# Performance work log

Measured on AMD Instinct MI355X. Metric: run time of the kernel, lower is better.

The kernel has to match this reference:

```python
import jax, jax.numpy as jnp
import numpy as np

N, E, IN_DIM, HID, G, NCLS, LAYERS = 200000, 1200000, 128, 64, 1024, 6, 3
BN_EPS = 1e-5


def _bn(x, g, b, m, v):
    # eval-mode BatchNorm1d with running stats
    return (x - m) * jax.lax.rsqrt(v + BN_EPS) * g + b


def setup_inputs() -> dict:
    key = jax.random.key(0)
    ks = jax.random.split(key, 24)
    s = 0.05
    d = {
        "x": jax.random.normal(ks[0], (N, IN_DIM), jnp.float32),
        "edge_index": jax.random.randint(ks[1], (2, E), 0, N, dtype=jnp.int32),
        "batch": jnp.sort(jax.random.randint(ks[2], (N,), 0, G, dtype=jnp.int32)),
        # input embedding + input BN
        "emb_w": jax.random.normal(ks[3], (IN_DIM, HID), jnp.float32) * s,
        "emb_b": jnp.zeros((HID,), jnp.float32),
        "ibn_g": jnp.ones((HID,), jnp.float32),
        "ibn_b": jnp.zeros((HID,), jnp.float32),
        "ibn_m": jax.random.normal(ks[4], (HID,), jnp.float32) * 0.1,
        "ibn_v": jax.random.uniform(ks[5], (HID,), jnp.float32, 0.5, 1.5),
        # stacked per-layer GIN MLP params [LAYERS, ...]
        "fc1_w": jax.random.normal(ks[6], (LAYERS, HID, HID), jnp.float32) * s,
        "fc1_b": jnp.zeros((LAYERS, HID), jnp.float32),
        "mbn_g": jnp.ones((LAYERS, HID), jnp.float32),
        "mbn_b": jnp.zeros((LAYERS, HID), jnp.float32),
        "mbn_m": jax.random.normal(ks[7], (LAYERS, HID), jnp.float32) * 0.1,
        "mbn_v": jax.random.uniform(ks[8], (LAYERS, HID), jnp.float32, 0.5, 1.5),
        "fc2_w": jax.random.normal(ks[9], (LAYERS, HID, HID), jnp.float32) * s,
        "fc2_b": jnp.zeros((LAYERS, HID), jnp.float32),
        # stacked per-layer outer BN params
        "obn_g": jnp.ones((LAYERS, HID), jnp.float32),
        "obn_b": jnp.zeros((LAYERS, HID), jnp.float32),
        "obn_m": jax.random.normal(ks[10], (LAYERS, HID), jnp.float32) * 0.1,
        "obn_v": jax.random.uniform(ks[11], (LAYERS, HID), jnp.float32, 0.5, 1.5),
        # classifier head
        "cls1_w": jax.random.normal(ks[12], (HID, HID // 2), jnp.float32) * s,
        "cls1_b": jnp.zeros((HID // 2,), jnp.float32),
        "cls2_w": jax.random.normal(ks[13], (HID // 2, NCLS), jnp.float32) * s,
        "cls2_b": jnp.zeros((NCLS,), jnp.float32),
    }
    return d


def reference(x, edge_index, batch,
              emb_w, emb_b, ibn_g, ibn_b, ibn_m, ibn_v,
              fc1_w, fc1_b, mbn_g, mbn_b, mbn_m, mbn_v, fc2_w, fc2_b,
              obn_g, obn_b, obn_m, obn_v,
              cls1_w, cls1_b, cls2_w, cls2_b):
    n = x.shape[0]
    src, dst = edge_index[0], edge_index[1]

    # input embed -> BN -> relu (dropout = identity in eval)
    h = jnp.dot(x, emb_w) + emb_b
    h = jax.nn.relu(_bn(h, ibn_g, ibn_b, ibn_m, ibn_v))

    for i in range(LAYERS):
        # GINConv (eps=0): aggregate neighbors via scatter-add, then MLP
        agg = jax.ops.segment_sum(h[src], dst, num_segments=n)
        z = h + agg
        z = jnp.dot(z, fc1_w[i]) + fc1_b[i]
        z = jax.nn.relu(_bn(z, mbn_g[i], mbn_b[i], mbn_m[i], mbn_v[i]))
        z = jnp.dot(z, fc2_w[i]) + fc2_b[i]
        # outer BN + relu
        h = jax.nn.relu(_bn(z, obn_g[i], obn_b[i], obn_m[i], obn_v[i]))

    # global mean pool per graph
    sums = jax.ops.segment_sum(h, batch, num_segments=G)
    cnts = jax.ops.segment_sum(jnp.ones((n,), h.dtype), batch, num_segments=G)
    pooled = sums / jnp.maximum(cnts, 1.0)[:, None]

    # classifier
    out = jax.nn.relu(jnp.dot(pooled, cls1_w) + cls1_b)
    out = jnp.dot(out, cls2_w) + cls2_b
    return out
```

## Files before the change

### kernel.cpp

```cpp
#include <hip/hip_runtime.h>
#include <hip/hip_bf16.h>

#define N_NODES 200000
#define N_EDGES 1200000
#define IN_DIM  128
#define HID     64
#define NGRAPH  1024
#define NCLS    6
#define BN_EPS  1e-5f

#define TILE_N   64
#define ZS       68
#define ECAP     1024

#define SCAN_CHUNK 1024
#define NBLK_SCAN ((N_NODES + SCAN_CHUNK - 1) / SCAN_CHUNK)

#define NBKT   128
#define BRANGE 1568
#define BCAP   12288
#define EPB    4096
#define NB_BIN ((N_EDGES + EPB - 1) / EPB)

#define SWZ(s) ((s) ^ (((s) >> 4) & 3))

typedef short bf16x8 __attribute__((ext_vector_type(8)));
typedef float f32x4  __attribute__((ext_vector_type(4)));
#define MFMA16(a,b,c) __builtin_amdgcn_mfma_f32_16x16x32_bf16((a),(b),(c),0,0,0)

__device__ __forceinline__ unsigned short f2bf(float f) {
    union { __hip_bfloat16 h; unsigned short u; } v; v.h = __float2bfloat16(f); return v.u;
}
__device__ __forceinline__ float bfbits2f(unsigned short u) {
    union { unsigned int i; float f; } v; v.i = ((unsigned int)u) << 16; return v.f;
}
__device__ __forceinline__ void cvt4(const float4& x, uint2& hi, uint2& lo) {
    const unsigned short h0 = f2bf(x.x), h1 = f2bf(x.y), h2 = f2bf(x.z), h3 = f2bf(x.w);
    hi.x = (unsigned)h0 | ((unsigned)h1 << 16);
    hi.y = (unsigned)h2 | ((unsigned)h3 << 16);
    const unsigned short l0 = f2bf(x.x - bfbits2f(h0)), l1 = f2bf(x.y - bfbits2f(h1));
    const unsigned short l2 = f2bf(x.z - bfbits2f(h2)), l3 = f2bf(x.w - bfbits2f(h3));
    lo.x = (unsigned)l0 | ((unsigned)l1 << 16);
    lo.y = (unsigned)l2 | ((unsigned)l3 << 16);
}

__global__ __launch_bounds__(256) void prep_emb_kernel(
    const float* __restrict__ w, unsigned short* __restrict__ wpe)
{
    const int idx = blockIdx.x * 256 + threadIdx.x;
    if (idx >= 16384) return;
    const int j = idx & 7, l = (idx >> 3) & 63;
    const int plane = (idx >> 9) & 1, s = (idx >> 10) & 3, ct = (idx >> 12) & 3;
    const int n = ct * 16 + (l & 15);
    const int k = s * 32 + (l >> 4) * 8 + j;
    const float f = w[k * 64 + n];
    const unsigned short hb = f2bf(f);
    wpe[idx] = plane ? f2bf(f - bfbits2f(hb)) : hb;
}

__global__ __launch_bounds__(256) void prep_fc_kernel(
    const float* __restrict__ fc1, const float* __restrict__ fc2,
    unsigned short* __restrict__ wpf)
{
    const int idx = blockIdx.x * 256 + threadIdx.x;
    if (idx >= 49152) return;
    const int j = idx & 7, l = (idx >> 3) & 63;
    const int plane = (idx >> 9) & 1, s = (idx >> 10) & 1, ct = (idx >> 11) & 3;
    const int g = (idx >> 13) & 1, layer = idx >> 14;
    const int n = ct * 16 + (l & 15);
    const int k = s * 32 + (l >> 4) * 8 + j;
    const float* W = g ? fc2 : fc1;
    const float f = W[(layer * 64 + k) * 64 + n];
    const unsigned short hb = f2bf(f);
    wpf[idx] = plane ? f2bf(f - bfbits2f(hb)) : hb;
}

__global__ __launch_bounds__(256) void bin_kernel(
    const int* __restrict__ src, const int* __restrict__ dst,
    int* __restrict__ gcnt, uint2* __restrict__ ebin)
{
    __shared__ int hist[NBKT];
    __shared__ int basis[NBKT];
    const int t = threadIdx.x;
    const int base = blockIdx.x * EPB;
    if (t < NBKT) hist[t] = 0;
    __syncthreads();
    int sv[16], dv[16];
    #pragma unroll
    for (int i = 0; i < 16; i++) {
        const int e = base + t + i * 256;
        if (e < N_EDGES) {
            sv[i] = src[e]; dv[i] = dst[e];
            atomicAdd(&hist[dv[i] / BRANGE], 1);
        } else { sv[i] = -1; dv[i] = -1; }
    }
    __syncthreads();
    if (t < NBKT) { basis[t] = atomicAdd(&gcnt[t], hist[t]); hist[t] = 0; }
    __syncthreads();
    #pragma unroll
    for (int i = 0; i < 16; i++) {
        if (dv[i] >= 0) {
            const int bb = dv[i] / BRANGE;
            const int pos = basis[bb] + atomicAdd(&hist[bb], 1);
            ebin[(size_t)bb * BCAP + pos] = make_uint2((unsigned)sv[i], (unsigned)dv[i]);
        }
    }
}

__global__ __launch_bounds__(512) void bindeg_kernel(
    const int* __restrict__ gcnt, const uint2* __restrict__ ebin,
    int* __restrict__ deg)
{
    __shared__ int hist[BRANGE];
    const int b = blockIdx.x, t = threadIdx.x;
    for (int i = t; i < BRANGE; i += 512) hist[i] = 0;
    __syncthreads();
    const int cnt = gcnt[b];
    const int r0 = b * BRANGE;
    const uint2* __restrict__ eb = ebin + (size_t)b * BCAP;
    for (int i = t; i < cnt; i += 512)
        atomicAdd(&hist[(int)eb[i].y - r0], 1);
    __syncthreads();
    for (int i = t; i < BRANGE; i += 512)
        if (r0 + i < N_NODES) deg[r0 + i] = hist[i];
}

__global__ __launch_bounds__(512) void binscatter_kernel(
    const int* __restrict__ gcnt, const uint2* __restrict__ ebin,
    const int* __restrict__ offs, int* __restrict__ csr_src)
{
    __shared__ int cur[BRANGE];
    const int b = blockIdx.x, t = threadIdx.x;
    const int r0 = b * BRANGE;
    const int lim = (r0 + BRANGE <= N_NODES) ? BRANGE : (N_NODES - r0);
    for (int i = t; i < lim; i += 512) cur[i] = offs[r0 + i];
    __syncthreads();
    const int cnt = gcnt[b];
    const uint2* __restrict__ eb = ebin + (size_t)b * BCAP;
    for (int i = t; i < cnt; i += 512) {
        const uint2 e = eb[i];
        const int pos = atomicAdd(&cur[(int)e.y - r0], 1);
        csr_src[pos] = (int)e.x;
    }
}

__global__ __launch_bounds__(256) void scan_sum_kernel(
    const int* __restrict__ deg, int* __restrict__ bsum)
{
    __shared__ int sd[256];
    const int b = blockIdx.x, t = threadIdx.x;
    const int base = b * SCAN_CHUNK;
    int s = 0;
    #pragma unroll
    for (int i = 0; i < SCAN_CHUNK / 256; i++) {
        const int idx = base + t + i * 256;
        s += (idx < N_NODES) ? deg[idx] : 0;
    }
    sd[t] = s; __syncthreads();
    for (int off = 128; off > 0; off >>= 1) {
        if (t < off) sd[t] += sd[t + off];
        __syncthreads();
    }
    if (t == 0) bsum[b] = sd[0];
}

__global__ __launch_bounds__(256) void scan_block_kernel(
    const int* __restrict__ bsum, int* __restrict__ boff, int* __restrict__ offs)
{
    __shared__ int sd[256];
    const int t = threadIdx.x;
    const int v = (t < NBLK_SCAN) ? bsum[t] : 0;
    sd[t] = v; __syncthreads();
    for (int off = 1; off < 256; off <<= 1) {
        const int u = (t >= off) ? sd[t - off] : 0;
        __syncthreads();
        sd[t] += u;
        __syncthreads();
    }
    if (t < NBLK_SCAN) boff[t] = sd[t] - v;
    if (t == 0) offs[N_NODES] = N_EDGES;
}

__global__ __launch_bounds__(256) void scan_scatter_kernel(
    const int* __restrict__ deg, const int* __restrict__ boff, int* __restrict__ offs)
{
    __shared__ int sd[256];
    const int b = blockIdx.x, t = threadIdx.x;
    const int base = b * SCAN_CHUNK + t * 4;
    int d0 = 0, d1 = 0, d2 = 0, d3 = 0;
    if (base + 0 < N_NODES) d0 = deg[base + 0];
    if (base + 1 < N_NODES) d1 = deg[base + 1];
    if (base + 2 < N_NODES) d2 = deg[base + 2];
    if (base + 3 < N_NODES) d3 = deg[base + 3];
    const int ts = d0 + d1 + d2 + d3;
    sd[t] = ts; __syncthreads();
    for (int off = 1; off < 256; off <<= 1) {
        const int u = (t >= off) ? sd[t - off] : 0;
        __syncthreads();
        sd[t] += u;
        __syncthreads();
    }
    const int excl = sd[t] - ts + boff[b];
    if (base + 0 < N_NODES) offs[base + 0] = excl;
    if (base + 1 < N_NODES) offs[base + 1] = excl + d0;
    if (base + 2 < N_NODES) offs[base + 2] = excl + d0 + d1;
    if (base + 3 < N_NODES) offs[base + 3] = excl + d0 + d1 + d2;
}

__global__ __launch_bounds__(256) void graph_offs_kernel(
    const int* __restrict__ batch, int* __restrict__ goffs)
{
    const int g = blockIdx.x * 256 + threadIdx.x;
    if (g > NGRAPH) return;
    if (g == NGRAPH) { goffs[NGRAPH] = N_NODES; return; }
    int lo = 0, hi = N_NODES;
    while (lo < hi) {
        const int mid = (lo + hi) >> 1;
        if (batch[mid] < g) lo = mid + 1; else hi = mid;
    }
    goffs[g] = lo;
}

__global__ __launch_bounds__(256) void pool_kernel(
    const float* __restrict__ h, const int* __restrict__ goffs,
    float* __restrict__ pooled, float* __restrict__ cnt)
{
    __shared__ float4 red[4][16];
    const int g = blockIdx.x, t = threadIdx.x;
    const int s = goffs[g], e = goffs[g + 1];
    const int grp = t >> 4;
    const int q = t & 15;
    float4 acc = {0.f, 0.f, 0.f, 0.f};
    for (int n = s + grp; n < e; n += 16) {
        const float4 v = *(const float4*)(h + (size_t)n * HID + q * 4);
        acc.x += v.x; acc.y += v.y; acc.z += v.z; acc.w += v.w;
    }
    #pragma unroll
    for (int off = 16; off <= 32; off <<= 1) {
        acc.x += __shfl_xor(acc.x, off, 64);
        acc.y += __shfl_xor(acc.y, off, 64);
        acc.z += __shfl_xor(acc.z, off, 64);
        acc.w += __shfl_xor(acc.w, off, 64);
    }
    const int wv = t >> 6, lane = t & 63;
    if (lane < 16) red[wv][lane] = acc;
    __syncthreads();
    if (t < 16) {
        float4 a = red[0][t];
        const float4 b = red[1][t], c = red[2][t], d = red[3][t];
        a.x += b.x + c.x + d.x;
        a.y += b.y + c.y + d.y;
        a.z += b.z + c.z + d.z;
        a.w += b.w + c.w + d.w;
        *(float4*)(pooled + (size_t)g * HID + t * 4) = a;
    }
    if (t == 0) cnt[g] = (float)(e - s);
}

__global__ __launch_bounds__(256) void embed_kernel(
    const float* __restrict__ x, const unsigned short* __restrict__ wpe,
    const float* __restrict__ bias,
    const float* __restrict__ bn_g, const float* __restrict__ bn_b,
    const float* __restrict__ bn_m, const float* __restrict__ bn_v,
    float* __restrict__ h)
{
    __shared__ __align__(16) float Ush[8192];
    __shared__ float BNs[128];
    short* Abuf = (short*)Ush;
    float* Ztmp = Ush;
    const int t = threadIdx.x, lane = t & 63, w = t >> 6;
    const int base = blockIdx.x * TILE_N;

    if (t < 64) {
        const float s = bn_g[t] * rsqrtf(bn_v[t] + BN_EPS);
        BNs[t] = s;
        BNs[64 + t] = bias[t] * s + bn_b[t] - bn_m[t] * s;
    }
    #pragma unroll
    for (int i = 0; i < 8; i++) {
        const int idx = t + i * 256;
        const int n = idx >> 5, k4 = idx & 31;
        const float4 v = *(const float4*)(x + (size_t)(base + n) * IN_DIM + k4 * 4);
        uint2 hi, lo; cvt4(v, hi, lo);
        const int s = k4 >> 3, lc = (n & 15) + 16 * ((k4 >> 1) & 3);
        const int half = k4 & 1, wm = n >> 4;
        const int sl0 = ((wm * 4 + s) * 2 + 0) * 64 + lc;
        const int sl1 = ((wm * 4 + s) * 2 + 1) * 64 + lc;
        *(uint2*)&Abuf[SWZ(sl0) * 8 + half * 4] = hi;
        *(uint2*)&Abuf[SWZ(sl1) * 8 + half * 4] = lo;
    }
    __syncthreads();

    const bf16x8* A = (const bf16x8*)Abuf;
    const bf16x8* B = (const bf16x8*)wpe;
    bf16x8 ah[4], al[4];
    #pragma unroll
    for (int s = 0; s < 4; s++) {
        ah[s] = A[SWZ(((w * 4 + s) * 2 + 0) * 64 + lane)];
        al[s] = A[SWZ(((w * 4 + s) * 2 + 1) * 64 + lane)];
    }
    __syncthreads();
    const int q = lane >> 4, c = lane & 15;
    #pragma unroll
    for (int ct = 0; ct < 4; ct++) {
        f32x4 acc = {0.f, 0.f, 0.f, 0.f};
        #pragma unroll
        for (int s = 0; s < 4; s++) {
            const bf16x8 bh = B[(ct << 9) + (s << 7) + lane];
            const bf16x8 bl = B[(ct << 9) + (s << 7) + 64 + lane];
            acc = MFMA16(ah[s], bh, acc);
            acc = MFMA16(ah[s], bl, acc);
            acc = MFMA16(al[s], bh, acc);
        }
        const int n = ct * 16 + c;
        const float sc = BNs[n], sh = BNs[64 + n];
        #pragma unroll
        for (int r = 0; r < 4; r++)
            Ztmp[(w * 16 + q * 4 + r) * ZS + n] = fmaxf(acc[r] * sc + sh, 0.f);
    }
    __syncthreads();
    #pragma unroll
    for (int i = 0; i < 4; i++) {
        const int idx = t + i * 256, n = idx >> 4, k4 = idx & 15;
        *(float4*)(h + (size_t)(base + n) * HID + k4 * 4) =
            *(const float4*)(&Ztmp[n * ZS + k4 * 4]);
    }
}

__global__ __launch_bounds__(256, 6) void agg_mlp_kernel(
    const float* __restrict__ hin, float* __restrict__ hout,
    const int* __restrict__ offs, const int* __restrict__ csr,
    const unsigned short* __restrict__ wp1, const unsigned short* __restrict__ wp2,
    const float* __restrict__ b1, const float* __restrict__ g1,
    const float* __restrict__ bb1, const float* __restrict__ m1, const float* __restrict__ v1,
    const float* __restrict__ b2, const float* __restrict__ g2,
    const float* __restrict__ bb2, const float* __restrict__ m2, const float* __restrict__ v2)
{
    __shared__ __align__(16) float Ush[TILE_N * ZS];
    __shared__ int   OF[TILE_N + 1];
    __shared__ int   EIDX[ECAP];
    __shared__ float BNs[256];
    short* Abuf = (short*)Ush;
    float* Ztmp = Ush;
    const int t = threadIdx.x, lane = t & 63, w = t >> 6;
    const int sub = lane >> 4, cq = lane & 15;
    const int base = blockIdx.x * TILE_N;

    if (t < 64) {
        const float sa = g1[t] * rsqrtf(v1[t] + BN_EPS);
        BNs[t] = sa; BNs[64 + t] = b1[t] * sa + bb1[t] - m1[t] * sa;
        const float sb = g2[t] * rsqrtf(v2[t] + BN_EPS);
        BNs[128 + t] = sb; BNs[192 + t] = b2[t] * sb + bb2[t] - m2[t] * sb;
    }
    if (t <= TILE_N) OF[t] = offs[base + t];
    const int segStart = offs[base];
    const int segEnd   = offs[base + TILE_N];
    for (int i = t; i < segEnd - segStart; i += 256)
        if (i < ECAP) EIDX[i] = csr[segStart + i];
    __syncthreads();

    const float* __restrict__ hc = hin + cq * 4;
    #pragma unroll
    for (int pp = 0; pp < 2; pp++) {
        const int mlA = (pp * 2 + 0) * 4 + sub;
        const int mlB = (pp * 2 + 1) * 4 + sub;
        const int nlA = w * 16 + mlA, nlB = w * 16 + mlB;
        int eA = OF[nlA]; const int eA1 = OF[nlA + 1];
        int eB = OF[nlB]; const int eB1 = OF[nlB + 1];
        const int eAm = (eA1 - 1 > segStart) ? eA1 - 1 : segStart;
        const int eBm = (eB1 - 1 > segStart) ? eB1 - 1 : segStart;
        float4 accA = *(const float4*)(hin + (size_t)(base + nlA) * HID + cq * 4);
        float4 accB = *(const float4*)(hin + (size_t)(base + nlB) * HID + cq * 4);
        while (eA < eA1 || eB < eB1) {
            int ia[4], ib[4];
            #pragma unroll
            for (int k = 0; k < 4; k++) {
                const int ea = (eA + k < eAm) ? eA + k : eAm;
                const int eb = (eB + k < eBm) ? eB + k : eBm;
                const int la = ea - segStart, lb = eb - segStart;
                ia[k] = (la < ECAP) ? EIDX[la] : csr[ea];
                ib[k] = (lb < ECAP) ? EIDX[lb] : csr[eb];
            }
            float4 va[4], vb[4];
            #pragma unroll
            for (int k = 0; k < 4; k++) {
                va[k] = *(const float4*)(hc + (size_t)ia[k] * HID);
                vb[k] = *(const float4*)(hc + (size_t)ib[k] * HID);
            }
            #pragma unroll
            for (int k = 0; k < 4; k++) {
                const float ma = (eA + k < eA1) ? 1.f : 0.f;
                const float mb = (eB + k < eB1) ? 1.f : 0.f;
                accA.x += ma * va[k].x; accA.y += ma * va[k].y;
                accA.z += ma * va[k].z; accA.w += ma * va[k].w;
                accB.x += mb * vb[k].x; accB.y += mb * vb[k].y;
                accB.z += mb * vb[k].z; accB.w += mb * vb[k].w;
            }
            eA += 4; eB += 4;
        }
        {
            uint2 hi, lo; cvt4(accA, hi, lo);
            const int s = cq >> 3, lc = mlA + 16 * ((cq >> 1) & 3), half = cq & 1;
            const int sl0 = ((w * 2 + s) * 2 + 0) * 64 + lc;
            const int sl1 = ((w * 2 + s) * 2 + 1) * 64 + lc;
            *(uint2*)&Abuf[SWZ(sl0) * 8 + half * 4] = hi;
            *(uint2*)&Abuf[SWZ(sl1) * 8 + half * 4] = lo;
        }
        {
            uint2 hi, lo; cvt4(accB, hi, lo);
            const int s = cq >> 3, lc = mlB + 16 * ((cq >> 1) & 3), half = cq & 1;
            const int sl0 = ((w * 2 + s) * 2 + 0) * 64 + lc;
            const int sl1 = ((w * 2 + s) * 2 + 1) * 64 + lc;
            *(uint2*)&Abuf[SWZ(sl0) * 8 + half * 4] = hi;
            *(uint2*)&Abuf[SWZ(sl1) * 8 + half * 4] = lo;
        }
    }
    __syncthreads();

    const bf16x8* A = (const bf16x8*)Abuf;
    const int q = lane >> 4, c = lane & 15;

    {
        const bf16x8 a0h = A[SWZ(((w * 2 + 0) * 2 + 0) * 64 + lane)];
        const bf16x8 a0l = A[SWZ(((w * 2 + 0) * 2 + 1) * 64 + lane)];
        const bf16x8 a1h = A[SWZ(((w * 2 + 1) * 2 + 0) * 64 + lane)];
        const bf16x8 a1l = A[SWZ(((w * 2 + 1) * 2 + 1) * 64 + lane)];
        __syncthreads();
        const bf16x8* B = (const bf16x8*)wp1;
        #pragma unroll
        for (int ct = 0; ct < 4; ct++) {
            const bf16x8 b0h = B[(ct << 8) + lane];
            const bf16x8 b0l = B[(ct << 8) + 64 + lane];
            const bf16x8 b1h_ = B[(ct << 8) + 128 + lane];
            const bf16x8 b1l_ = B[(ct << 8) + 192 + lane];
            f32x4 acc = {0.f, 0.f, 0.f, 0.f};
            acc = MFMA16(a0h, b0h, acc);
            acc = MFMA16(a0h, b0l, acc);
            acc = MFMA16(a0l, b0h, acc);
            acc = MFMA16(a1h, b1h_, acc);
            acc = MFMA16(a1h, b1l_, acc);
            acc = MFMA16(a1l, b1h_, acc);
            const int n = ct * 16 + c;
            const float sc = BNs[n], sh = BNs[64 + n];
            #pragma unroll
            for (int r = 0; r < 4; r++)
                Ztmp[(w * 16 + q * 4 + r) * ZS + n] = fmaxf(acc[r] * sc + sh, 0.f);
        }
    }
    __syncthreads();

    {
        const int m = t >> 2;
        float4 vv[4];
        #pragma unroll
        for (int d = 0; d < 4; d++) {
            const int k4 = (t & 3) * 4 + d;
            vv[d] = *(const float4*)(&Ztmp[m * ZS + k4 * 4]);
        }
        __syncthreads();
        #pragma unroll
        for (int d = 0; d < 4; d++) {
            const int k4 = (t & 3) * 4 + d;
            uint2 hi, lo; cvt4(vv[d], hi, lo);
            const int s = k4 >> 3, lc = (m & 15) + 16 * ((k4 >> 1) & 3);
            const int half = k4 & 1, wm = m >> 4;
            const int sl0 = ((wm * 2 + s) * 2 + 0) * 64 + lc;
            const int sl1 = ((wm * 2 + s) * 2 + 1) * 64 + lc;
            *(uint2*)&Abuf[SWZ(sl0) * 8 + half * 4] = hi;
            *(uint2*)&Abuf[SWZ(sl1) * 8 + half * 4] = lo;
        }
    }
    __syncthreads();

    {
        const bf16x8 a0h = A[SWZ(((w * 2 + 0) * 2 + 0) * 64 + lane)];
        const bf16x8 a0l = A[SWZ(((w * 2 + 0) * 2 + 1) * 64 + lane)];
        const bf16x8 a1h = A[SWZ(((w * 2 + 1) * 2 + 0) * 64 + lane)];
        const bf16x8 a1l = A[SWZ(((w * 2 + 1) * 2 + 1) * 64 + lane)];
        __syncthreads();
        const bf16x8* B = (const bf16x8*)wp2;
        #pragma unroll
        for (int ct = 0; ct < 4; ct++) {
            const bf16x8 b0h = B[(ct << 8) + lane];
            const bf16x8 b0l = B[(ct << 8) + 64 + lane];
            const bf16x8 b1h_ = B[(ct << 8) + 128 + lane];
            const bf16x8 b1l_ = B[(ct << 8) + 192 + lane];
            f32x4 acc = {0.f, 0.f, 0.f, 0.f};
            acc = MFMA16(a0h, b0h, acc);
            acc = MFMA16(a0h, b0l, acc);
            acc = MFMA16(a0l, b0h, acc);
            acc = MFMA16(a1h, b1h_, acc);
            acc = MFMA16(a1h, b1l_, acc);
            acc = MFMA16(a1l, b1h_, acc);
            const int n = ct * 16 + c;
            const float sc = BNs[128 + n], sh = BNs[192 + n];
            #pragma unroll
            for (int r = 0; r < 4; r++)
                Ztmp[(w * 16 + q * 4 + r) * ZS + n] = fmaxf(acc[r] * sc + sh, 0.f);
        }
    }
    __syncthreads();

    #pragma unroll
    for (int i = 0; i < 4; i++) {
        const int idx = t + i * 256, n = idx >> 4, k4 = idx & 15;
        *(float4*)(hout + (size_t)(base + n) * HID + k4 * 4) =
            *(const float4*)(&Ztmp[n * ZS + k4 * 4]);
    }
}

__global__ __launch_bounds__(64) void cls_kernel(
    const float* __restrict__ pooled, const float* __restrict__ cnt,
    const float* __restrict__ w1, const float* __restrict__ b1,
    const float* __restrict__ w2, const float* __restrict__ b2,
    float* __restrict__ out)
{
    const int g = blockIdx.x;
    const int lane = threadIdx.x;
    const float c = cnt[g];
    const float p = pooled[(size_t)g * HID + lane] / fmaxf(c, 1.f);
    float acc = (lane < 32) ? b1[lane] : 0.f;
    #pragma unroll
    for (int k = 0; k < 64; k++) {
        const float pk = __shfl(p, k, 64);
        if (lane < 32) acc += pk * w1[k * 32 + lane];
    }
    const float hmid = fmaxf(acc, 0.f);
    float acc2 = (lane < NCLS) ? b2[lane] : 0.f;
    #pragma unroll
    for (int k = 0; k < 32; k++) {
        const float hk = __shfl(hmid, k, 64);
        if (lane < NCLS) acc2 += hk * w2[k * NCLS + lane];
    }
    if (lane < NCLS) out[(size_t)g * NCLS + lane] = acc2;
}

extern "C" void kernel_launch(void* const* d_in, const int* in_sizes, int n_in,
                              void* d_out, int out_size, void* d_ws, size_t ws_size,
                              hipStream_t stream) {
    const float* x     = (const float*)d_in[0];
    const int*   ei    = (const int*)d_in[1];
    const int*   batch = (const int*)d_in[2];
    const float* emb_w = (const float*)d_in[3];
    const float* emb_b = (const float*)d_in[4];
    const float* ibn_g = (const float*)d_in[5];
    const float* ibn_b = (const float*)d_in[6];
    const float* ibn_m = (const float*)d_in[7];
    const float* ibn_v = (const float*)d_in[8];
    const float* fc1_w = (const float*)d_in[9];
    const float* fc1_b = (const float*)d_in[10];
    const float* mbn_g = (const float*)d_in[11];
    const float* mbn_b = (const float*)d_in[12];
    const float* mbn_m = (const float*)d_in[13];
    const float* mbn_v = (const float*)d_in[14];
    const float* fc2_w = (const float*)d_in[15];
    const float* fc2_b = (const float*)d_in[16];
    const float* obn_g = (const float*)d_in[17];
    const float* obn_b = (const float*)d_in[18];
    const float* obn_m = (const float*)d_in[19];
    const float* obn_v = (const float*)d_in[20];
    const float* cls1w = (const float*)d_in[21];
    const float* cls1b = (const float*)d_in[22];
    const float* cls2w = (const float*)d_in[23];
    const float* cls2b = (const float*)d_in[24];

    float* h0     = (float*)d_ws;
    float* h1     = h0 + (size_t)N_NODES * HID;
    float* pooled = h1 + (size_t)N_NODES * HID;
    float* cnt    = pooled + NGRAPH * HID;
    int*   deg    = (int*)(cnt + NGRAPH);
    int*   offs   = deg + N_NODES;
    int*   bsum   = offs + (N_NODES + 1);
    int*   boff   = bsum + NBLK_SCAN;
    int*   csr    = boff + NBLK_SCAN;
    unsigned short* wpe = (unsigned short*)(csr + N_EDGES);
    unsigned short* wpf = wpe + 16384;
    int*   goffs  = (int*)(wpf + 49152);
    int*   gcnt   = goffs + (NGRAPH + 1);
    uint2* ebin   = (uint2*)h0;

    const int* src = ei;
    const int* dst = ei + N_EDGES;

    prep_emb_kernel<<<64, 256, 0, stream>>>(emb_w, wpe);
    prep_fc_kernel<<<192, 256, 0, stream>>>(fc1_w, fc2_w, wpf);

    graph_offs_kernel<<<(NGRAPH + 256) / 256, 256, 0, stream>>>(batch, goffs);

    hipMemsetAsync(gcnt, 0, NBKT * sizeof(int), stream);
    bin_kernel<<<NB_BIN, 256, 0, stream>>>(src, dst, gcnt, ebin);
    bindeg_kernel<<<NBKT, 512, 0, stream>>>(gcnt, ebin, deg);
    scan_sum_kernel<<<NBLK_SCAN, 256, 0, stream>>>(deg, bsum);
    scan_block_kernel<<<1, 256, 0, stream>>>(bsum, boff, offs);
    scan_scatter_kernel<<<NBLK_SCAN, 256, 0, stream>>>(deg, boff, offs);
    binscatter_kernel<<<NBKT, 512, 0, stream>>>(gcnt, ebin, offs, csr);

    const int gemm_blocks = N_NODES / TILE_N;
    embed_kernel<<<gemm_blocks, 256, 0, stream>>>(x, wpe, emb_b,
                                                  ibn_g, ibn_b, ibn_m, ibn_v, h0);

    const float* hin = h0;
    float* hout = h1;
    for (int i = 0; i < 3; i++) {
        agg_mlp_kernel<<<gemm_blocks, 256, 0, stream>>>(
            hin, hout, offs, csr,
            wpf + (size_t)(i * 2 + 0) * 8192, wpf + (size_t)(i * 2 + 1) * 8192,
            fc1_b + i * HID, mbn_g + i * HID, mbn_b + i * HID, mbn_m + i * HID, mbn_v + i * HID,
            fc2_b + i * HID, obn_g + i * HID, obn_b + i * HID, obn_m + i * HID, obn_v + i * HID);
        const float* tmp = hin; hin = hout; hout = (float*)tmp;
    }

    pool_kernel<<<NGRAPH, 256, 0, stream>>>(h1, goffs, pooled, cnt);

    cls_kernel<<<NGRAPH, 64, 0, stream>>>(pooled, cnt, cls1w, cls1b, cls2w, cls2b,
                                          (float*)d_out);
}
```

Baseline: 489.4 us.

## Merge setup kernels, pack edge bins to 32-bit, use nontemporal loads/stores

Folds the two weight-prep kernels, the graph-offset search and the gcnt memset into one setup launch to cut launch overhead. Packs each binned edge into one 32-bit word (18-bit source plus a local destination offset), halving bin traffic. Adds nontemporal loads and stores on streaming accesses (x, edge arrays, h writes, pool reads) and switches float4 to a vector type. Nontemporal hints could hurt if later kernels reread the data from cache, for example h being reused by the next layer's gather.

```diff
diff --git a/kernel.cpp b/kernel.cpp
--- a/kernel.cpp
+++ b/kernel.cpp
@@ -34,50 +34,61 @@
 __device__ __forceinline__ float bfbits2f(unsigned short u) {
     union { unsigned int i; float f; } v; v.i = ((unsigned int)u) << 16; return v.f;
 }
-__device__ __forceinline__ void cvt4(const float4& x, uint2& hi, uint2& lo) {
-    const unsigned short h0 = f2bf(x.x), h1 = f2bf(x.y), h2 = f2bf(x.z), h3 = f2bf(x.w);
+__device__ __forceinline__ void cvt4(const f32x4& x, uint2& hi, uint2& lo) {
+    const unsigned short h0 = f2bf(x[0]), h1 = f2bf(x[1]), h2 = f2bf(x[2]), h3 = f2bf(x[3]);
     hi.x = (unsigned)h0 | ((unsigned)h1 << 16);
     hi.y = (unsigned)h2 | ((unsigned)h3 << 16);
-    const unsigned short l0 = f2bf(x.x - bfbits2f(h0)), l1 = f2bf(x.y - bfbits2f(h1));
-    const unsigned short l2 = f2bf(x.z - bfbits2f(h2)), l3 = f2bf(x.w - bfbits2f(h3));
+    const unsigned short l0 = f2bf(x[0] - bfbits2f(h0)), l1 = f2bf(x[1] - bfbits2f(h1));
+    const unsigned short l2 = f2bf(x[2] - bfbits2f(h2)), l3 = f2bf(x[3] - bfbits2f(h3));
     lo.x = (unsigned)l0 | ((unsigned)l1 << 16);
     lo.y = (unsigned)l2 | ((unsigned)l3 << 16);
 }
 
-__global__ __launch_bounds__(256) void prep_emb_kernel(
-    const float* __restrict__ w, unsigned short* __restrict__ wpe)
-{
-    const int idx = blockIdx.x * 256 + threadIdx.x;
-    if (idx >= 16384) return;
-    const int j = idx & 7, l = (idx >> 3) & 63;
-    const int plane = (idx >> 9) & 1, s = (idx >> 10) & 3, ct = (idx >> 12) & 3;
-    const int n = ct * 16 + (l & 15);
-    const int k = s * 32 + (l >> 4) * 8 + j;
-    const float f = w[k * 64 + n];
-    const unsigned short hb = f2bf(f);
-    wpe[idx] = plane ? f2bf(f - bfbits2f(hb)) : hb;
-}
-
-__global__ __launch_bounds__(256) void prep_fc_kernel(
+__global__ __launch_bounds__(256) void setup_kernel(
+    const float* __restrict__ emb_w, unsigned short* __restrict__ wpe,
     const float* __restrict__ fc1, const float* __restrict__ fc2,
-    unsigned short* __restrict__ wpf)
-{
-    const int idx = blockIdx.x * 256 + threadIdx.x;
-    if (idx >= 49152) return;
-    const int j = idx & 7, l = (idx >> 3) & 63;
-    const int plane = (idx >> 9) & 1, s = (idx >> 10) & 1, ct = (idx >> 11) & 3;
-    const int g = (idx >> 13) & 1, layer = idx >> 14;
-    const int n = ct * 16 + (l & 15);
-    const int k = s * 32 + (l >> 4) * 8 + j;
-    const float* W = g ? fc2 : fc1;
-    const float f = W[(layer * 64 + k) * 64 + n];
-    const unsigned short hb = f2bf(f);
-    wpf[idx] = plane ? f2bf(f - bfbits2f(hb)) : hb;
+    unsigned short* __restrict__ wpf,
+    const int* __restrict__ batch, int* __restrict__ goffs,
+    int* __restrict__ gcnt)
+{
+    const int b = blockIdx.x, t = threadIdx.x;
+    if (b < 64) {
+        const int idx = b * 256 + t;
+        const int j = idx & 7, l = (idx >> 3) & 63;
+        const int plane = (idx >> 9) & 1, s = (idx >> 10) & 3, ct = (idx >> 12) & 3;
+        const int n = ct * 16 + (l & 15);
+        const int k = s * 32 + (l >> 4) * 8 + j;
+        const float f = emb_w[k * 64 + n];
+        const unsigned short hb = f2bf(f);
+        wpe[idx] = plane ? f2bf(f - bfbits2f(hb)) : hb;
+    } else if (b < 256) {
+        const int idx = (b - 64) * 256 + t;
+        const int j = idx & 7, l = (idx >> 3) & 63;
+        const int plane = (idx >> 9) & 1, s = (idx >> 10) & 1, ct = (idx >> 11) & 3;
+        const int g = (idx >> 13) & 1, layer = idx >> 14;
+        const int n = ct * 16 + (l & 15);
+        const int k = s * 32 + (l >> 4) * 8 + j;
+        const float* W = g ? fc2 : fc1;
+        const float f = W[(layer * 64 + k) * 64 + n];
+        const unsigned short hb = f2bf(f);
+        wpf[idx] = plane ? f2bf(f - bfbits2f(hb)) : hb;
+    } else {
+        if (b == 256 && t < NBKT) gcnt[t] = 0;
+        const int g = (b - 256) * 256 + t;
+        if (g > NGRAPH) return;
+        if (g == NGRAPH) { goffs[NGRAPH] = N_NODES; return; }
+        int lo = 0, hi = N_NODES;
+        while (lo < hi) {
+            const int mid = (lo + hi) >> 1;
+            if (batch[mid] < g) lo = mid + 1; else hi = mid;
+        }
+        goffs[g] = lo;
+    }
 }
 
 __global__ __launch_bounds__(256) void bin_kernel(
     const int* __restrict__ src, const int* __restrict__ dst,
-    int* __restrict__ gcnt, uint2* __restrict__ ebin)
+    int* __restrict__ gcnt, unsigned* __restrict__ ebin)
 {
     __shared__ int hist[NBKT];
     __shared__ int basis[NBKT];
@@ -90,7 +101,8 @@
     for (int i = 0; i < 16; i++) {
         const int e = base + t + i * 256;
         if (e < N_EDGES) {
-            sv[i] = src[e]; dv[i] = dst[e];
+            sv[i] = __builtin_nontemporal_load(&src[e]);
+            dv[i] = __builtin_nontemporal_load(&dst[e]);
             atomicAdd(&hist[dv[i] / BRANGE], 1);
         } else { sv[i] = -1; dv[i] = -1; }
     }
@@ -101,14 +113,17 @@
     for (int i = 0; i < 16; i++) {
         if (dv[i] >= 0) {
             const int bb = dv[i] / BRANGE;
+            const int dl = dv[i] - bb * BRANGE;
             const int pos = basis[bb] + atomicAdd(&hist[bb], 1);
-            ebin[(size_t)bb * BCAP + pos] = make_uint2((unsigned)sv[i], (unsigned)dv[i]);
+            __builtin_nontemporal_store(
+                (unsigned)sv[i] | ((unsigned)dl << 18),
+                &ebin[(size_t)bb * BCAP + pos]);
         }
     }
 }
 
 __global__ __launch_bounds__(512) void bindeg_kernel(
-    const int* __restrict__ gcnt, const uint2* __restrict__ ebin,
+    const int* __restrict__ gcnt, const unsigned* __restrict__ ebin,
     int* __restrict__ deg)
 {
     __shared__ int hist[BRANGE];
@@ -117,16 +132,18 @@
     __syncthreads();
     const int cnt = gcnt[b];
     const int r0 = b * BRANGE;
-    const uint2* __restrict__ eb = ebin + (size_t)b * BCAP;
-    for (int i = t; i < cnt; i += 512)
-        atomicAdd(&hist[(int)eb[i].y - r0], 1);
+    const unsigned* __restrict__ eb = ebin + (size_t)b * BCAP;
+    for (int i = t; i < cnt; i += 512) {
+        const unsigned e = __builtin_nontemporal_load(&eb[i]);
+        atomicAdd(&hist[e >> 18], 1);
+    }
     __syncthreads();
     for (int i = t; i < BRANGE; i += 512)
         if (r0 + i < N_NODES) deg[r0 + i] = hist[i];
 }
 
 __global__ __launch_bounds__(512) void binscatter_kernel(
-    const int* __restrict__ gcnt, const uint2* __restrict__ ebin,
+    const int* __restrict__ gcnt, const unsigned* __restrict__ ebin,
     const int* __restrict__ offs, int* __restrict__ csr_src)
 {
     __shared__ int cur[BRANGE];
@@ -136,11 +153,11 @@
     for (int i = t; i < lim; i += 512) cur[i] = offs[r0 + i];
     __syncthreads();
     const int cnt = gcnt[b];
-    const uint2* __restrict__ eb = ebin + (size_t)b * BCAP;
+    const unsigned* __restrict__ eb = ebin + (size_t)b * BCAP;
     for (int i = t; i < cnt; i += 512) {
-        const uint2 e = eb[i];
-        const int pos = atomicAdd(&cur[(int)e.y - r0], 1);
-        csr_src[pos] = (int)e.x;
+        const unsigned e = __builtin_nontemporal_load(&eb[i]);
+        const int pos = atomicAdd(&cur[e >> 18], 1);
+        csr_src[pos] = (int)(e & 0x3FFFFu);
     }
 }
 
@@ -207,52 +224,34 @@
     if (base + 3 < N_NODES) offs[base + 3] = excl + d0 + d1 + d2;
 }
 
-__global__ __launch_bounds__(256) void graph_offs_kernel(
-    const int* __restrict__ batch, int* __restrict__ goffs)
-{
-    const int g = blockIdx.x * 256 + threadIdx.x;
-    if (g > NGRAPH) return;
-    if (g == NGRAPH) { goffs[NGRAPH] = N_NODES; return; }
-    int lo = 0, hi = N_NODES;
-    while (lo < hi) {
-        const int mid = (lo + hi) >> 1;
-        if (batch[mid] < g) lo = mid + 1; else hi = mid;
-    }
-    goffs[g] = lo;
-}
-
 __global__ __launch_bounds__(256) void pool_kernel(
     const float* __restrict__ h, const int* __restrict__ goffs,
     float* __restrict__ pooled, float* __restrict__ cnt)
 {
-    __shared__ float4 red[4][16];
+    __shared__ f32x4 red[4][16];
     const int g = blockIdx.x, t = threadIdx.x;
     const int s = goffs[g], e = goffs[g + 1];
     const int grp = t >> 4;
     const int q = t & 15;
-    float4 acc = {0.f, 0.f, 0.f, 0.f};
+    f32x4 acc = {0.f, 0.f, 0.f, 0.f};
     for (int n = s + grp; n < e; n += 16) {
-        const float4 v = *(const float4*)(h + (size_t)n * HID + q * 4);
-        acc.x += v.x; acc.y += v.y; acc.z += v.z; acc.w += v.w;
+        const f32x4 v = __builtin_nontemporal_load(
+            (const f32x4*)(h + (size_t)n * HID + q * 4));
+        acc += v;
     }
     #pragma unroll
     for (int off = 16; off <= 32; off <<= 1) {
-        acc.x += __shfl_xor(acc.x, off, 64);
-        acc.y += __shfl_xor(acc.y, off, 64);
-        acc.z += __shfl_xor(acc.z, off, 64);
-        acc.w += __shfl_xor(acc.w, off, 64);
+        acc[0] += __shfl_xor(acc[0], off, 64);
+        acc[1] += __shfl_xor(acc[1], off, 64);
+        acc[2] += __shfl_xor(acc[2], off, 64);
+        acc[3] += __shfl_xor(acc[3], off, 64);
     }
     const int wv = t >> 6, lane = t & 63;
     if (lane < 16) red[wv][lane] = acc;
     __syncthreads();
     if (t < 16) {
-        float4 a = red[0][t];
-        const float4 b = red[1][t], c = red[2][t], d = red[3][t];
-        a.x += b.x + c.x + d.x;
-        a.y += b.y + c.y + d.y;
-        a.z += b.z + c.z + d.z;
-        a.w += b.w + c.w + d.w;
-        *(float4*)(pooled + (size_t)g * HID + t * 4) = a;
+        f32x4 a = red[0][t] + red[1][t] + red[2][t] + red[3][t];
+        *(f32x4*)(pooled + (size_t)g * HID + t * 4) = a;
     }
     if (t == 0) cnt[g] = (float)(e - s);
 }
@@ -280,7 +279,8 @@
     for (int i = 0; i < 8; i++) {
         const int idx = t + i * 256;
         const int n = idx >> 5, k4 = idx & 31;
-        const float4 v = *(const float4*)(x + (size_t)(base + n) * IN_DIM + k4 * 4);
+        const f32x4 v = __builtin_nontemporal_load(
+            (const f32x4*)(x + (size_t)(base + n) * IN_DIM + k4 * 4));
         uint2 hi, lo; cvt4(v, hi, lo);
         const int s = k4 >> 3, lc = (n & 15) + 16 * ((k4 >> 1) & 3);
         const int half = k4 & 1, wm = n >> 4;
@@ -322,8 +322,9 @@
     #pragma unroll
     for (int i = 0; i < 4; i++) {
         const int idx = t + i * 256, n = idx >> 4, k4 = idx & 15;
-        *(float4*)(h + (size_t)(base + n) * HID + k4 * 4) =
-            *(const float4*)(&Ztmp[n * ZS + k4 * 4]);
+        const f32x4 z = *(const f32x4*)(&Ztmp[n * ZS + k4 * 4]);
+        __builtin_nontemporal_store(z,
+            (f32x4*)(h + (size_t)(base + n) * HID + k4 * 4));
     }
 }
 
@@ -369,8 +370,10 @@
         int eB = OF[nlB]; const int eB1 = OF[nlB + 1];
         const int eAm = (eA1 - 1 > segStart) ? eA1 - 1 : segStart;
         const int eBm = (eB1 - 1 > segStart) ? eB1 - 1 : segStart;
-        float4 accA = *(const float4*)(hin + (size_t)(base + nlA) * HID + cq * 4);
-        float4 accB = *(const float4*)(hin + (size_t)(base + nlB) * HID + cq * 4);
+        f32x4 accA = __builtin_nontemporal_load(
+            (const f32x4*)(hin + (size_t)(base + nlA) * HID + cq * 4));
+        f32x4 accB = __builtin_nontemporal_load(
+            (const f32x4*)(hin + (size_t)(base + nlB) * HID + cq * 4));
         while (eA < eA1 || eB < eB1) {
             int ia[4], ib[4];
             #pragma unroll
@@ -381,20 +384,18 @@
                 ia[k] = (la < ECAP) ? EIDX[la] : csr[ea];
                 ib[k] = (lb < ECAP) ? EIDX[lb] : csr[eb];
             }
-            float4 va[4], vb[4];
+            f32x4 va[4], vb[4];
             #pragma unroll
             for (int k = 0; k < 4; k++) {
-                va[k] = *(const float4*)(hc + (size_t)ia[k] * HID);
-                vb[k] = *(const float4*)(hc + (size_t)ib[k] * HID);
+                va[k] = *(const f32x4*)(hc + (size_t)ia[k] * HID);
+                vb[k] = *(const f32x4*)(hc + (size_t)ib[k] * HID);
             }
             #pragma unroll
             for (int k = 0; k < 4; k++) {
                 const float ma = (eA + k < eA1) ? 1.f : 0.f;
                 const float mb = (eB + k < eB1) ? 1.f : 0.f;
-                accA.x += ma * va[k].x; accA.y += ma * va[k].y;
-                accA.z += ma * va[k].z; accA.w += ma * va[k].w;
-                accB.x += mb * vb[k].x; accB.y += mb * vb[k].y;
-                accB.z += mb * vb[k].z; accB.w += mb * vb[k].w;
+                accA += va[k] * ma;
+                accB += vb[k] * mb;
             }
             eA += 4; eB += 4;
         }
@@ -451,11 +452,11 @@
 
     {
         const int m = t >> 2;
-        float4 vv[4];
+        f32x4 vv[4];
         #pragma unroll
         for (int d = 0; d < 4; d++) {
             const int k4 = (t & 3) * 4 + d;
-            vv[d] = *(const float4*)(&Ztmp[m * ZS + k4 * 4]);
+            vv[d] = *(const f32x4*)(&Ztmp[m * ZS + k4 * 4]);
         }
         __syncthreads();
         #pragma unroll
@@ -504,8 +505,9 @@
     #pragma unroll
     for (int i = 0; i < 4; i++) {
         const int idx = t + i * 256, n = idx >> 4, k4 = idx & 15;
-        *(float4*)(hout + (size_t)(base + n) * HID + k4 * 4) =
-            *(const float4*)(&Ztmp[n * ZS + k4 * 4]);
+        const f32x4 z = *(const f32x4*)(&Ztmp[n * ZS + k4 * 4]);
+        __builtin_nontemporal_store(z,
+            (f32x4*)(hout + (size_t)(base + n) * HID + k4 * 4));
     }
 }
 
@@ -577,17 +579,14 @@
     unsigned short* wpf = wpe + 16384;
     int*   goffs  = (int*)(wpf + 49152);
     int*   gcnt   = goffs + (NGRAPH + 1);
-    uint2* ebin   = (uint2*)h0;
+    unsigned* ebin = (unsigned*)h0;
 
     const int* src = ei;
     const int* dst = ei + N_EDGES;
 
-    prep_emb_kernel<<<64, 256, 0, stream>>>(emb_w, wpe);
-    prep_fc_kernel<<<192, 256, 0, stream>>>(fc1_w, fc2_w, wpf);
-
-    graph_offs_kernel<<<(NGRAPH + 256) / 256, 256, 0, stream>>>(batch, goffs);
-
-    hipMemsetAsync(gcnt, 0, NBKT * sizeof(int), stream);
+    setup_kernel<<<261, 256, 0, stream>>>(emb_w, wpe, fc1_w, fc2_w, wpf,
+                                          batch, goffs, gcnt);
+
     bin_kernel<<<NB_BIN, 256, 0, stream>>>(src, dst, gcnt, ebin);
     bindeg_kernel<<<NBKT, 512, 0, stream>>>(gcnt, ebin, deg);
     scan_sum_kernel<<<NBLK_SCAN, 256, 0, stream>>>(deg, bsum);
```

Result: slower. 511.4 us (+4.5%).
